# Optimization experiments

Measured on AMD Instinct MI355X. Metric: run time of the kernel, lower is better.

Reference implementation:

```python
import jax, jax.numpy as jnp
import numpy as np

B, T, C, H = 8, 2048, 384, 64

def setup_inputs() -> dict:
    key = jax.random.key(0)
    k1, k2, k3, k4 = jax.random.split(key, 4)
    x = jax.random.normal(k1, (B, T, C), dtype=jnp.float32)
    Wq = jax.random.normal(k2, (C, H), dtype=jnp.float32) * (C ** -0.5)
    Wk = jax.random.normal(k3, (C, H), dtype=jnp.float32) * (C ** -0.5)
    Wv = jax.random.normal(k4, (C, H), dtype=jnp.float32) * (C ** -0.5)
    return {"x": x, "Wq": Wq, "Wk": Wk, "Wv": Wv}

def reference(x, Wq, Wk, Wv):
    # x: (B, T, C); projections: (B, T, H)
    Bn, Tn, Cn = x.shape
    q = jnp.einsum('btc,ch->bth', x, Wq)
    k = jnp.einsum('btc,ch->bth', x, Wk)
    v = jnp.einsum('btc,ch->bth', x, Wv)
    # NOTE: source scales by C**-0.5 (embedding dim), not head_size**-0.5
    weights = jnp.einsum('bth,bsh->bts', q, k) * (Cn ** -0.5)  # (B, T, T)
    causal = jnp.tril(jnp.ones((Tn, Tn), dtype=bool))
    weights = jnp.where(causal, weights, -jnp.inf)
    # NOTE: source applies softmax over dim=1 (query/row axis), reproduced faithfully
    weights = jax.nn.softmax(weights, axis=1)
    # dropout omitted (eval-mode reference)
    return jnp.einsum('bts,bsh->bth', weights, v)
```

## Files before the change

kernel.cpp:

```cpp
#include <hip/hip_runtime.h>
#include <hip/hip_bf16.h>
#include <math.h>

#define Bn 8
#define Tn 2048
#define Cn 384
#define Hn 64
#define SCALE 0.051031036307982884f

using bf16x8 = __attribute__((ext_vector_type(8))) short;
using f32x4  = __attribute__((ext_vector_type(4))) float;

#define MFMA(a, b, c) __builtin_amdgcn_mfma_f32_16x16x32_bf16((a), (b), (c), 0, 0, 0)

static __device__ __forceinline__ short f2bf(float f) {
  unsigned u = __float_as_uint(f);
  u += 0x7fffu + ((u >> 16) & 1u);
  return (short)(u >> 16);
}
static __device__ __forceinline__ float bf2f(short s) {
  return __uint_as_float(((unsigned)(unsigned short)s) << 16);
}

__global__ __launch_bounds__(256) void wconv_kernel(
    const float* __restrict__ Wq, const float* __restrict__ Wk,
    const float* __restrict__ Wv, short* __restrict__ WbT) {
  int idx = blockIdx.x * 256 + threadIdx.x;
  int n = idx / 384, k = idx - n * 384;
  const float* W = (n < 64) ? Wq : (n < 128) ? Wk : Wv;
  WbT[idx] = f2bf(W[k * 64 + (n & 63)]);
}

__global__ __launch_bounds__(256) void proj_kernel(
    const float* __restrict__ x, const short* __restrict__ WbT,
    short* __restrict__ qb, short* __restrict__ kb, short* __restrict__ vT) {
  __shared__ short xs[16][392];
  __shared__ short vtile[64][20];
  const int tid = threadIdx.x;
  const int t0 = blockIdx.x * 16;
  const float* xb = x + (size_t)t0 * Cn;
  #pragma unroll
  for (int i = 0; i < 6; ++i) {
    int j = tid + i * 256;
    int row = j / 96, colv = (j - row * 96) * 4;
    float4 v = *(const float4*)(xb + row * Cn + colv);
    short4 s4; s4.x = f2bf(v.x); s4.y = f2bf(v.y); s4.z = f2bf(v.z); s4.w = f2bf(v.w);
    *(short4*)(&xs[row][colv]) = s4;
  }
  __syncthreads();
  const int w = tid >> 6, l15 = tid & 15, quad = (tid & 63) >> 4;
  f32x4 acc[3] = {};
  for (int ks = 0; ks < 12; ++ks) {
    bf16x8 a = *(const bf16x8*)(&xs[l15][ks * 32 + quad * 8]);
    #pragma unroll
    for (int cf = 0; cf < 3; ++cf) {
      bf16x8 bfr = *(const bf16x8*)(WbT + (size_t)(48 * w + 16 * cf + l15) * Cn + ks * 32 + quad * 8);
      acc[cf] = MFMA(a, bfr, acc[cf]);
    }
  }
  #pragma unroll
  for (int cf = 0; cf < 3; ++cf) {
    int cbase = 48 * w + 16 * cf, c = cbase + l15;
    #pragma unroll
    for (int r = 0; r < 4; ++r) {
      int row = t0 + quad * 4 + r;
      short val = f2bf(acc[cf][r]);
      if (cbase < 64)       qb[(size_t)row * Hn + c] = val;
      else if (cbase < 128) kb[(size_t)row * Hn + (c - 64)] = val;
      else                  vtile[c - 128][quad * 4 + r] = val;
    }
  }
  __syncthreads();
  const int b = t0 >> 11, t0l = t0 & 2047;
  int h = tid >> 2, tseg = (tid & 3) * 4;
  *(short4*)(vT + ((size_t)(b * Hn + h)) * Tn + t0l + tseg) =
      *(const short4*)(&vtile[h][tseg]);
}

__global__ __launch_bounds__(256) void colstats_kernel(
    const short* __restrict__ qb, const short* __restrict__ kb,
    float* __restrict__ L, short* __restrict__ Eb) {
  const int unit = blockIdx.x;
  const int b = unit >> 7, rem = unit & 127;
  const int j = rem >> 3, u = rem & 7;
  const int lo = (u * 33) >> 3, hi = ((u + 1) * 33) >> 3;
  const int big = 32 - j;
  const int tid = threadIdx.x, w = tid >> 6, l15 = tid & 15, quad = (tid & 63) >> 4;
  const size_t Ebase = (size_t)b * Tn * Tn;
  __shared__ float redl[64][17];

  auto run = [&](const int i, const int k0, const int k1) {
    if (k0 >= k1) return;
    const int s0 = i << 6;
    bf16x8 bk[8];
    #pragma unroll
    for (int nf = 0; nf < 4; ++nf) {
      const size_t krow = (size_t)(b * Tn + s0 + 16 * nf + l15) * Hn;
      bk[2 * nf]     = *(const bf16x8*)(kb + krow + quad * 8);
      bk[2 * nf + 1] = *(const bf16x8*)(kb + krow + 32 + quad * 8);
    }
    float l[4] = {0.f, 0.f, 0.f, 0.f};
    auto cload = [&](bf16x8& A0, bf16x8& A1, int k) {
      size_t ar = (size_t)(b * Tn + ((i + k) << 6) + 16 * w + l15) * Hn;
      A0 = *(const bf16x8*)(qb + ar + quad * 8);
      A1 = *(const bf16x8*)(qb + ar + 32 + quad * 8);
    };
    auto ccomp = [&](bf16x8 A0, bf16x8 A1, int k) {
      f32x4 sc[4] = {};
      #pragma unroll
      for (int nf = 0; nf < 4; ++nf) {
        sc[nf] = MFMA(A0, bk[2 * nf], sc[nf]);
        sc[nf] = MFMA(A1, bk[2 * nf + 1], sc[nf]);
      }
      const bool diag = (k == 0);
      const int tb = ((i + k) << 6) + 16 * w + quad * 4;
      #pragma unroll
      for (int nf = 0; nf < 4; ++nf) {
        int s = s0 + 16 * nf + l15;
        #pragma unroll
        for (int r = 0; r < 4; ++r) {
          float v = sc[nf][r] * SCALE;
          if (diag && (tb + r) < s) v = -INFINITY;
          float ev = __expf(v);
          l[nf] += ev;
          Eb[Ebase + (size_t)(tb + r) * Tn + s] = f2bf(ev);
        }
      }
    };
    bf16x8 a0A, a1A, a0B, a1B;
    cload(a0A, a1A, k0);
    int k = k0;
    while (k + 1 < k1) {
      cload(a0B, a1B, k + 1);
      ccomp(a0A, a1A, k);
      if (k + 2 < k1) cload(a0A, a1A, k + 2);
      ccomp(a0B, a1B, k + 1);
      k += 2;
    }
    if (k < k1) ccomp(a0A, a1A, k);
    __syncthreads();
    #pragma unroll
    for (int nf = 0; nf < 4; ++nf) redl[16 * nf + l15][w * 4 + quad] = l[nf];
    __syncthreads();
    if (tid < 64) {
      float ls = 0.f;
      #pragma unroll
      for (int q2 = 0; q2 < 16; ++q2) ls += redl[tid][q2];
      atomicAdd(&L[b * Tn + s0 + tid], ls);
    }
  };
  run(j, lo, min(hi, big));
  run(31 - j, max(lo, big) - big, hi - big);
}

__global__ __launch_bounds__(256) void vhat_kernel(
    const short* __restrict__ vT, const float* __restrict__ L,
    short* __restrict__ vS) {
  int gid = blockIdx.x * 256 + threadIdx.x;
  size_t base = (size_t)gid * 8;
  int b = (int)(base >> 17), s = (int)(base & 2047);
  short4 v0 = *(const short4*)(vT + base);
  short4 v1 = *(const short4*)(vT + base + 4);
  const float* Lp = L + b * Tn + s;
  float4 L0 = *(const float4*)(Lp);
  float4 L1 = *(const float4*)(Lp + 4);
  short4 r0, r1;
  r0.x = f2bf(bf2f(v0.x) / L0.x); r0.y = f2bf(bf2f(v0.y) / L0.y);
  r0.z = f2bf(bf2f(v0.z) / L0.z); r0.w = f2bf(bf2f(v0.w) / L0.w);
  r1.x = f2bf(bf2f(v1.x) / L1.x); r1.y = f2bf(bf2f(v1.y) / L1.y);
  r1.z = f2bf(bf2f(v1.z) / L1.z); r1.w = f2bf(bf2f(v1.w) / L1.w);
  *(short4*)(vS + base) = r0;
  *(short4*)(vS + base + 4) = r1;
}

__global__ __launch_bounds__(256) void outg_kernel(
    const short* __restrict__ Eb, const short* __restrict__ vS,
    float* __restrict__ out) {
  const int g = blockIdx.x;
  const int tile = 31 - (g >> 3), b = g & 7;
  const int tid = threadIdx.x, w = tid >> 6, l15 = tid & 15, quad = (tid & 63) >> 4;
  const int tbase = (tile << 6) + 16 * w;
  const size_t Abase = (size_t)b * Tn * Tn + (size_t)(tbase + l15) * Tn;
  const size_t Bbase = (size_t)b * Hn * Tn;
  f32x4 acc[4] = {};
  const int nch = tile + 1;
  bf16x8 aA[2], bA[8], aB[2], bB[8];
  auto load = [&](bf16x8 (&A)[2], bf16x8 (&Bf)[8], int ch) {
    const int s0 = ch << 6;
    A[0] = *(const bf16x8*)(Eb + Abase + s0 + quad * 8);
    A[1] = *(const bf16x8*)(Eb + Abase + s0 + 32 + quad * 8);
    #pragma unroll
    for (int nf = 0; nf < 4; ++nf) {
      const size_t br = Bbase + (size_t)(16 * nf + l15) * Tn + s0;
      Bf[2 * nf]     = *(const bf16x8*)(vS + br + quad * 8);
      Bf[2 * nf + 1] = *(const bf16x8*)(vS + br + 32 + quad * 8);
    }
  };
  auto comp = [&](bf16x8 (&A)[2], bf16x8 (&Bf)[8]) {
    #pragma unroll
    for (int nf = 0; nf < 4; ++nf) {
      acc[nf] = MFMA(A[0], Bf[2 * nf], acc[nf]);
      acc[nf] = MFMA(A[1], Bf[2 * nf + 1], acc[nf]);
    }
  };
  load(aA, bA, 0);
  int ch = 0;
  while (ch + 1 < nch) {
    load(aB, bB, ch + 1);
    comp(aA, bA);
    if (ch + 2 < nch) load(aA, bA, ch + 2);
    comp(aB, bB);
    ch += 2;
  }
  if (ch < nch) comp(aA, bA);
  #pragma unroll
  for (int nf = 0; nf < 4; ++nf)
    #pragma unroll
    for (int r = 0; r < 4; ++r)
      out[(size_t)(b * Tn + tbase + quad * 4 + r) * Hn + 16 * nf + l15] = acc[nf][r];
}

extern "C" void kernel_launch(void* const* d_in, const int* in_sizes, int n_in,
                              void* d_out, int out_size, void* d_ws, size_t ws_size,
                              hipStream_t stream) {
  const float* x  = (const float*)d_in[0];
  const float* Wq = (const float*)d_in[1];
  const float* Wk = (const float*)d_in[2];
  const float* Wv = (const float*)d_in[3];
  char* ws = (char*)d_ws;
  short* qb   = (short*)(ws);
  short* kb   = (short*)(ws + 2097152);
  short* vT   = (short*)(ws + 4194304);
  short* vS   = (short*)(ws + 6291456);
  short* WbT  = (short*)(ws + 8388608);
  float* L    = (float*)(ws + 8536064);
  short* Eb   = (short*)(ws + 16777216);
  float* outp = (float*)d_out;

  hipMemsetAsync(L, 0, (size_t)Bn * Tn * 4, stream);
  hipLaunchKernelGGL(wconv_kernel, dim3(288), dim3(256), 0, stream, Wq, Wk, Wv, WbT);
  hipLaunchKernelGGL(proj_kernel, dim3(Bn * Tn / 16), dim3(256), 0, stream, x, WbT, qb, kb, vT);
  hipLaunchKernelGGL(colstats_kernel, dim3(1024), dim3(256), 0, stream, qb, kb, L, Eb);
  hipLaunchKernelGGL(vhat_kernel, dim3(512), dim3(256), 0, stream, vT, L, vS);
  hipLaunchKernelGGL(outg_kernel, dim3(256), dim3(256), 0, stream, Eb, vS, outp);
}
```

Measured before the change: 153.8 us.

## Tile colstats and output GEMM over lower-triangular 128x128 blocks with atomics

Both the score/exp kernel and the output GEMM now assign one 128x128 (t,s) tile of the causal lower triangle to each block, giving 136 tiles per batch. The score kernel loads Q and K fragments once per tile instead of streaming 64-row chunks. The output kernel splits along the key dimension and accumulates partial results into the output with fp32 atomicAdd, which needs an extra memset of the output. The goal is better load balance and more parallelism than the old 256-block row-tile output kernel, whose per-block work varied with the diagonal. The cost is many global atomics on the output and the loss of the explicit double-buffered load pipelining.

```diff
diff --git a/kernel.cpp b/kernel.cpp
--- a/kernel.cpp
+++ b/kernel.cpp
@@ -80,77 +80,62 @@
 __global__ __launch_bounds__(256) void colstats_kernel(
     const short* __restrict__ qb, const short* __restrict__ kb,
     float* __restrict__ L, short* __restrict__ Eb) {
-  const int unit = blockIdx.x;
-  const int b = unit >> 7, rem = unit & 127;
-  const int j = rem >> 3, u = rem & 7;
-  const int lo = (u * 33) >> 3, hi = ((u + 1) * 33) >> 3;
-  const int big = 32 - j;
+  const int g = blockIdx.x;
+  const int b = g / 136;
+  const int r = g - b * 136;
+  int ti = 0;
+  while (((ti + 1) * (ti + 2)) >> 1 <= r) ++ti;
+  const int si = r - ((ti * (ti + 1)) >> 1);
+  const int t0 = ti << 7, s0 = si << 7;
   const int tid = threadIdx.x, w = tid >> 6, l15 = tid & 15, quad = (tid & 63) >> 4;
+  const int wt = w >> 1, ws = w & 1;
   const size_t Ebase = (size_t)b * Tn * Tn;
-  __shared__ float redl[64][17];
-
-  auto run = [&](const int i, const int k0, const int k1) {
-    if (k0 >= k1) return;
-    const int s0 = i << 6;
-    bf16x8 bk[8];
+  __shared__ float redl[128][9];
+
+  f32x4 acc[4][4] = {};
+  #pragma unroll
+  for (int ks = 0; ks < 2; ++ks) {
+    bf16x8 A[4], Bf[4];
+    #pragma unroll
+    for (int mf = 0; mf < 4; ++mf)
+      A[mf] = *(const bf16x8*)(qb + (size_t)(b * Tn + t0 + wt * 64 + mf * 16 + l15) * Hn + ks * 32 + quad * 8);
+    #pragma unroll
+    for (int nf = 0; nf < 4; ++nf)
+      Bf[nf] = *(const bf16x8*)(kb + (size_t)(b * Tn + s0 + ws * 64 + nf * 16 + l15) * Hn + ks * 32 + quad * 8);
+    #pragma unroll
+    for (int mf = 0; mf < 4; ++mf)
+      #pragma unroll
+      for (int nf = 0; nf < 4; ++nf)
+        acc[mf][nf] = MFMA(A[mf], Bf[nf], acc[mf][nf]);
+  }
+  const bool diag = (si == ti);
+  float colsum[4] = {0.f, 0.f, 0.f, 0.f};
+  #pragma unroll
+  for (int mf = 0; mf < 4; ++mf) {
+    const int tb = t0 + wt * 64 + mf * 16 + quad * 4;
     #pragma unroll
     for (int nf = 0; nf < 4; ++nf) {
-      const size_t krow = (size_t)(b * Tn + s0 + 16 * nf + l15) * Hn;
-      bk[2 * nf]     = *(const bf16x8*)(kb + krow + quad * 8);
-      bk[2 * nf + 1] = *(const bf16x8*)(kb + krow + 32 + quad * 8);
-    }
-    float l[4] = {0.f, 0.f, 0.f, 0.f};
-    auto cload = [&](bf16x8& A0, bf16x8& A1, int k) {
-      size_t ar = (size_t)(b * Tn + ((i + k) << 6) + 16 * w + l15) * Hn;
-      A0 = *(const bf16x8*)(qb + ar + quad * 8);
-      A1 = *(const bf16x8*)(qb + ar + 32 + quad * 8);
-    };
-    auto ccomp = [&](bf16x8 A0, bf16x8 A1, int k) {
-      f32x4 sc[4] = {};
-      #pragma unroll
-      for (int nf = 0; nf < 4; ++nf) {
-        sc[nf] = MFMA(A0, bk[2 * nf], sc[nf]);
-        sc[nf] = MFMA(A1, bk[2 * nf + 1], sc[nf]);
+      const int s = s0 + ws * 64 + nf * 16 + l15;
+      #pragma unroll
+      for (int r4 = 0; r4 < 4; ++r4) {
+        float v = acc[mf][nf][r4] * SCALE;
+        if (diag && s > tb + r4) v = -INFINITY;
+        float ev = __expf(v);
+        colsum[nf] += ev;
+        Eb[Ebase + (size_t)(tb + r4) * Tn + s] = f2bf(ev);
       }
-      const bool diag = (k == 0);
-      const int tb = ((i + k) << 6) + 16 * w + quad * 4;
-      #pragma unroll
-      for (int nf = 0; nf < 4; ++nf) {
-        int s = s0 + 16 * nf + l15;
-        #pragma unroll
-        for (int r = 0; r < 4; ++r) {
-          float v = sc[nf][r] * SCALE;
-          if (diag && (tb + r) < s) v = -INFINITY;
-          float ev = __expf(v);
-          l[nf] += ev;
-          Eb[Ebase + (size_t)(tb + r) * Tn + s] = f2bf(ev);
-        }
-      }
-    };
-    bf16x8 a0A, a1A, a0B, a1B;
-    cload(a0A, a1A, k0);
-    int k = k0;
-    while (k + 1 < k1) {
-      cload(a0B, a1B, k + 1);
-      ccomp(a0A, a1A, k);
-      if (k + 2 < k1) cload(a0A, a1A, k + 2);
-      ccomp(a0B, a1B, k + 1);
-      k += 2;
-    }
-    if (k < k1) ccomp(a0A, a1A, k);
-    __syncthreads();
-    #pragma unroll
-    for (int nf = 0; nf < 4; ++nf) redl[16 * nf + l15][w * 4 + quad] = l[nf];
-    __syncthreads();
-    if (tid < 64) {
-      float ls = 0.f;
-      #pragma unroll
-      for (int q2 = 0; q2 < 16; ++q2) ls += redl[tid][q2];
-      atomicAdd(&L[b * Tn + s0 + tid], ls);
-    }
-  };
-  run(j, lo, min(hi, big));
-  run(31 - j, max(lo, big) - big, hi - big);
+    }
+  }
+  #pragma unroll
+  for (int nf = 0; nf < 4; ++nf)
+    redl[ws * 64 + nf * 16 + l15][wt * 4 + quad] = colsum[nf];
+  __syncthreads();
+  if (tid < 128) {
+    float ls = 0.f;
+    #pragma unroll
+    for (int j = 0; j < 8; ++j) ls += redl[tid][j];
+    atomicAdd(&L[b * Tn + s0 + tid], ls);
+  }
 }
 
 __global__ __launch_bounds__(256) void vhat_kernel(
@@ -177,47 +162,44 @@
     const short* __restrict__ Eb, const short* __restrict__ vS,
     float* __restrict__ out) {
   const int g = blockIdx.x;
-  const int tile = 31 - (g >> 3), b = g & 7;
+  const int b = g / 136;
+  const int r = g - b * 136;
+  int ti = 0;
+  while (((ti + 1) * (ti + 2)) >> 1 <= r) ++ti;
+  const int si = r - ((ti * (ti + 1)) >> 1);
+  const int t0 = ti << 7, s0 = si << 7;
   const int tid = threadIdx.x, w = tid >> 6, l15 = tid & 15, quad = (tid & 63) >> 4;
-  const int tbase = (tile << 6) + 16 * w;
-  const size_t Abase = (size_t)b * Tn * Tn + (size_t)(tbase + l15) * Tn;
-  const size_t Bbase = (size_t)b * Hn * Tn;
-  f32x4 acc[4] = {};
-  const int nch = tile + 1;
-  bf16x8 aA[2], bA[8], aB[2], bB[8];
-  auto load = [&](bf16x8 (&A)[2], bf16x8 (&Bf)[8], int ch) {
-    const int s0 = ch << 6;
-    A[0] = *(const bf16x8*)(Eb + Abase + s0 + quad * 8);
-    A[1] = *(const bf16x8*)(Eb + Abase + s0 + 32 + quad * 8);
-    #pragma unroll
-    for (int nf = 0; nf < 4; ++nf) {
-      const size_t br = Bbase + (size_t)(16 * nf + l15) * Tn + s0;
-      Bf[2 * nf]     = *(const bf16x8*)(vS + br + quad * 8);
-      Bf[2 * nf + 1] = *(const bf16x8*)(vS + br + 32 + quad * 8);
-    }
-  };
-  auto comp = [&](bf16x8 (&A)[2], bf16x8 (&Bf)[8]) {
-    #pragma unroll
-    for (int nf = 0; nf < 4; ++nf) {
-      acc[nf] = MFMA(A[0], Bf[2 * nf], acc[nf]);
-      acc[nf] = MFMA(A[1], Bf[2 * nf + 1], acc[nf]);
-    }
-  };
-  load(aA, bA, 0);
-  int ch = 0;
-  while (ch + 1 < nch) {
-    load(aB, bB, ch + 1);
-    comp(aA, bA);
-    if (ch + 2 < nch) load(aA, bA, ch + 2);
-    comp(aB, bB);
-    ch += 2;
-  }
-  if (ch < nch) comp(aA, bA);
-  #pragma unroll
-  for (int nf = 0; nf < 4; ++nf)
-    #pragma unroll
-    for (int r = 0; r < 4; ++r)
-      out[(size_t)(b * Tn + tbase + quad * 4 + r) * Hn + 16 * nf + l15] = acc[nf][r];
+  const int wt = w >> 1, wh = w & 1;
+  const size_t Ebase = (size_t)b * Tn * Tn;
+  const size_t Vbase = (size_t)b * Hn * Tn;
+
+  f32x4 acc[4][2] = {};
+  #pragma unroll
+  for (int ks = 0; ks < 4; ++ks) {
+    bf16x8 A[4], Bf[2];
+    #pragma unroll
+    for (int mf = 0; mf < 4; ++mf)
+      A[mf] = *(const bf16x8*)(Eb + Ebase + (size_t)(t0 + wt * 64 + mf * 16 + l15) * Tn + s0 + ks * 32 + quad * 8);
+    #pragma unroll
+    for (int nf = 0; nf < 2; ++nf)
+      Bf[nf] = *(const bf16x8*)(vS + Vbase + (size_t)(wh * 32 + nf * 16 + l15) * Tn + s0 + ks * 32 + quad * 8);
+    #pragma unroll
+    for (int mf = 0; mf < 4; ++mf)
+      #pragma unroll
+      for (int nf = 0; nf < 2; ++nf)
+        acc[mf][nf] = MFMA(A[mf], Bf[nf], acc[mf][nf]);
+  }
+  #pragma unroll
+  for (int mf = 0; mf < 4; ++mf) {
+    const int tb = t0 + wt * 64 + mf * 16 + quad * 4;
+    #pragma unroll
+    for (int nf = 0; nf < 2; ++nf) {
+      const int h = wh * 32 + nf * 16 + l15;
+      #pragma unroll
+      for (int r4 = 0; r4 < 4; ++r4)
+        atomicAdd(&out[(size_t)(b * Tn + tb + r4) * Hn + h], acc[mf][nf][r4]);
+    }
+  }
 }
 
 extern "C" void kernel_launch(void* const* d_in, const int* in_sizes, int n_in,
@@ -238,9 +220,10 @@
   float* outp = (float*)d_out;
 
   hipMemsetAsync(L, 0, (size_t)Bn * Tn * 4, stream);
+  hipMemsetAsync(outp, 0, (size_t)Bn * Tn * Hn * 4, stream);
   hipLaunchKernelGGL(wconv_kernel, dim3(288), dim3(256), 0, stream, Wq, Wk, Wv, WbT);
   hipLaunchKernelGGL(proj_kernel, dim3(Bn * Tn / 16), dim3(256), 0, stream, x, WbT, qb, kb, vT);
-  hipLaunchKernelGGL(colstats_kernel, dim3(1024), dim3(256), 0, stream, qb, kb, L, Eb);
+  hipLaunchKernelGGL(colstats_kernel, dim3(Bn * 136), dim3(256), 0, stream, qb, kb, L, Eb);
   hipLaunchKernelGGL(vhat_kernel, dim3(512), dim3(256), 0, stream, vT, L, vS);
-  hipLaunchKernelGGL(outg_kernel, dim3(256), dim3(256), 0, stream, Eb, vS, outp);
-}
+  hipLaunchKernelGGL(outg_kernel, dim3(Bn * 136), dim3(256), 0, stream, Eb, vS, outp);
+}
```

After: 159.4 us. 3.6% more time.
